# Kernel optimization log

Hardware: AMD Instinct MI355X
Metric: run time of the kernel (lower is better)

Reference implementation:

```python
import jax, jax.numpy as jnp
import numpy as np

EMBED_DIM = 1024
TASK_BIAS_DIM = 128
BATCH = 4
SEQ = 2048


def setup_inputs() -> dict:
    key = jax.random.key(0)
    kq, kk, kv, kt, kw, kb = jax.random.split(key, 6)
    query = jax.random.normal(kq, (BATCH, SEQ, EMBED_DIM), dtype=jnp.float32)
    key_t = jax.random.normal(kk, (BATCH, SEQ, EMBED_DIM), dtype=jnp.float32)
    value = jax.random.normal(kv, (BATCH, SEQ, EMBED_DIM), dtype=jnp.float32)
    task_bias = jax.random.normal(kt, (BATCH, TASK_BIAS_DIM), dtype=jnp.float32)
    # task_bias_proj: Linear(task_bias_dim, 1) -> weight [1, task_bias_dim], bias [1]
    lim = 1.0 / np.sqrt(TASK_BIAS_DIM)
    W = jax.random.uniform(kw, (TASK_BIAS_DIM, 1), jnp.float32, -lim, lim)
    b = jax.random.uniform(kb, (1,), jnp.float32, -lim, lim)
    return {"query": query, "key": key_t, "value": value,
            "task_bias": task_bias, "W": W, "b": b}


def reference(query, key, value, task_bias, W, b):
    scale = EMBED_DIM ** 0.5
    # scores: [batch, seq, seq]
    scores = jnp.einsum('bqd,bkd->bqk', query, key) / scale
    # per-batch scalar gate from task bias: [batch, 1]
    gate = jax.nn.sigmoid(task_bias @ W + b)           # [batch, 1]
    scores = scores * gate[:, :, None]                 # broadcast [b,1,1]
    attention_weights = jax.nn.softmax(scores, axis=-1)
    output = jnp.einsum('bqk,bkd->bqd', attention_weights, value)
    return output, attention_weights
```

## Files before the change

### kernel.cpp

```cpp
#include <hip/hip_runtime.h>
#include <hip/hip_bf16.h>
#include <stdint.h>
#include <stddef.h>

#define B_  4
#define S_  2048
#define D_  1024
#define TB_ 128

typedef float v4f  __attribute__((ext_vector_type(4)));
typedef short s16x4 __attribute__((ext_vector_type(4)));
typedef short s16x8 __attribute__((ext_vector_type(8)));

#define WAITV(n) asm volatile("s_waitcnt vmcnt(" #n ")" ::: "memory")

__device__ __forceinline__ unsigned short f2bf(float f) {
  union { float f; unsigned u; } x; x.f = f;
  unsigned u = x.u;
  unsigned r = (u + 0x7FFFu + ((u >> 16) & 1u)) >> 16;
  return (unsigned short)r;
}

__device__ __forceinline__ void gld16(const void* g, void* l) {
  __builtin_amdgcn_global_load_lds(
      (const __attribute__((address_space(1))) unsigned int*)g,
      (__attribute__((address_space(3))) unsigned int*)l, 16, 0, 0);
}

__device__ __forceinline__ void barrier_sync() {
  asm volatile("" ::: "memory");
  __builtin_amdgcn_s_barrier();
  asm volatile("" ::: "memory");
  __builtin_amdgcn_sched_barrier(0);
}

__global__ __launch_bounds__(256) void gate_kernel(
    const float* __restrict__ tb, const float* __restrict__ W,
    const float* __restrict__ bias, float* __restrict__ gate) {
  int t = threadIdx.x;
  int b = t >> 6, l = t & 63;
  float s = tb[b * TB_ + l] * W[l] + tb[b * TB_ + 64 + l] * W[64 + l];
  #pragma unroll
  for (int off = 32; off > 0; off >>= 1) s += __shfl_down(s, off, 64);
  if (l == 0) gate[b] = 1.0f / (1.0f + __expf(-(s + bias[0])));
}

__global__ __launch_bounds__(256) void cvt_bf16_kernel(
    const float* __restrict__ src, short* __restrict__ dst) {
  size_t g = (size_t)blockIdx.x * 256 + threadIdx.x;
  v4f v = *(const v4f*)(src + g * 4);
  s16x4 o;
  o[0] = (short)f2bf(v[0]); o[1] = (short)f2bf(v[1]);
  o[2] = (short)f2bf(v[2]); o[3] = (short)f2bf(v[3]);
  *(s16x4*)(dst + g * 4) = o;
}

__global__ __launch_bounds__(256) void vT_kernel(
    const float* __restrict__ V, short* __restrict__ VT) {
  __shared__ float tile[64][65];
  int b = blockIdx.z;
  int s0 = blockIdx.x * 64, d0 = blockIdx.y * 64;
  int t = threadIdx.x;
  int tc = t & 63, tr4 = t >> 6;
  const float* src = V + ((size_t)b * S_ + s0) * D_ + d0;
  #pragma unroll
  for (int p = 0; p < 16; ++p) {
    int r = p * 4 + tr4;
    tile[r][tc] = src[(size_t)r * D_ + tc];
  }
  __syncthreads();
  short* dst = VT + ((size_t)b * D_ + d0) * S_ + s0;
  #pragma unroll
  for (int p = 0; p < 16; ++p) {
    int r = p * 4 + tr4;
    dst[(size_t)r * S_ + tc] = (short)f2bf(tile[tc][r]);
  }
}

template<int BN, int KTOT, int BROWS, int LDC, bool GATED>
__global__ __launch_bounds__(512, 2) void gemm_pipe(
    const short* __restrict__ Ag, const short* __restrict__ Bg,
    const float* __restrict__ gate, float* __restrict__ Cg) {
  extern __shared__ char lds[];
  constexpr int NF = BN / 64;
  constexpr int NT = KTOT / 64;
  constexpr int ABYTES = 256 * 128;
  constexpr int BBYTES = BN * 128;
  constexpr int BUFB = ABYTES + BBYTES;

  int wg = blockIdx.x;
  int swz = (wg & 7) * 32 + (wg >> 3);
  int b = swz >> 6;
  int rem = swz & 63;
  int m0 = (rem >> 3) * 256;
  int n0 = (rem & 7) * BN;

  int tid = threadIdx.x;
  int w = tid >> 6, l = tid & 63;
  int wm = w >> 2, wn = w & 3;

  const short* Ab = Ag + (size_t)b * S_ * KTOT + (size_t)m0 * KTOT;
  const short* Bb = Bg + (size_t)b * BROWS * KTOT + (size_t)n0 * KTOT;

  int srow8 = l >> 3;
  int schunk = ((l & 7) ^ srow8) * 8;

  int arow = wm * 128 + (l & 15);
  int brow = wn * (BN / 4) + (l & 15);
  int hi = l >> 4;
  int sl0 = (((0 + hi) ^ (l & 7)) * 16);
  int sl1 = (((4 + hi) ^ (l & 7)) * 16);

  v4f acc[8][NF];
  #pragma unroll
  for (int m = 0; m < 8; ++m)
    #pragma unroll
    for (int n = 0; n < NF; ++n)
      #pragma unroll
      for (int j = 0; j < 4; ++j) acc[m][n][j] = 0.0f;

  auto stage = [&](int t, int buf) {
    char* La = lds + buf * BUFB;
    char* Lb = La + ABYTES;
    const short* As = Ab + (size_t)t * 64 + schunk;
    #pragma unroll
    for (int j = 0; j < 4; ++j) {
      int blk = w * 4 + j;
      gld16(As + (size_t)(blk * 8 + srow8) * KTOT, La + blk * 1024);
    }
    const short* Bs = Bb + (size_t)t * 64 + schunk;
    #pragma unroll
    for (int j = 0; j < NF; ++j) {
      int blk = w * NF + j;
      gld16(Bs + (size_t)(blk * 8 + srow8) * KTOT, Lb + blk * 1024);
    }
  };

  auto compute = [&](int buf) {
    const char* La = lds + buf * BUFB + arow * 128;
    const char* Lb = lds + buf * BUFB + ABYTES + brow * 128;
    s16x8 bf0[NF], bf1[NF];
    #pragma unroll
    for (int n = 0; n < NF; ++n) {
      bf0[n] = *(const s16x8*)(Lb + n * 2048 + sl0);
      bf1[n] = *(const s16x8*)(Lb + n * 2048 + sl1);
    }
    #pragma unroll
    for (int mh = 0; mh < 2; ++mh) {
      s16x8 af[4];
      #pragma unroll
      for (int i = 0; i < 4; ++i)
        af[i] = *(const s16x8*)(La + (mh * 4 + i) * 2048 + sl0);
      __builtin_amdgcn_s_setprio(1);
      #pragma unroll
      for (int i = 0; i < 4; ++i)
        #pragma unroll
        for (int n = 0; n < NF; ++n)
          acc[mh * 4 + i][n] = __builtin_amdgcn_mfma_f32_16x16x32_bf16(
              af[i], bf0[n], acc[mh * 4 + i][n], 0, 0, 0);
      __builtin_amdgcn_s_setprio(0);
      #pragma unroll
      for (int i = 0; i < 4; ++i)
        af[i] = *(const s16x8*)(La + (mh * 4 + i) * 2048 + sl1);
      __builtin_amdgcn_s_setprio(1);
      #pragma unroll
      for (int i = 0; i < 4; ++i)
        #pragma unroll
        for (int n = 0; n < NF; ++n)
          acc[mh * 4 + i][n] = __builtin_amdgcn_mfma_f32_16x16x32_bf16(
              af[i], bf1[n], acc[mh * 4 + i][n], 0, 0, 0);
      __builtin_amdgcn_s_setprio(0);
    }
  };

  stage(0, 0);
  int cur = 0;
  for (int t = 0; t < NT - 1; ++t) {
    stage(t + 1, cur ^ 1);
    if constexpr (BN == 256) { WAITV(8); } else { WAITV(6); }
    barrier_sync();
    compute(cur);
    barrier_sync();
    cur ^= 1;
  }
  WAITV(0);
  barrier_sync();
  compute(cur);

  float g = 1.0f;
  if constexpr (GATED) g = gate[b] * 0.03125f;
  float* Cb = Cg + (size_t)b * S_ * LDC +
              (size_t)(m0 + wm * 128) * LDC + n0 + wn * (BN / 4);
  #pragma unroll
  for (int mf = 0; mf < 8; ++mf)
    #pragma unroll
    for (int n = 0; n < NF; ++n) {
      int r0 = mf * 16 + hi * 4;
      int c = n * 16 + (l & 15);
      #pragma unroll
      for (int j = 0; j < 4; ++j)
        Cb[(size_t)(r0 + j) * LDC + c] = acc[mf][n][j] * g;
    }
}

__global__ __launch_bounds__(256) void softmax_kernel(
    float* __restrict__ attn, short* __restrict__ attnb) {
  size_t row = blockIdx.x;
  float* p = attn + row * S_;
  int t = threadIdx.x;
  v4f v0 = *(const v4f*)(p + t * 8);
  v4f v1 = *(const v4f*)(p + t * 8 + 4);
  float m = fmaxf(fmaxf(fmaxf(v0[0], v0[1]), fmaxf(v0[2], v0[3])),
                  fmaxf(fmaxf(v1[0], v1[1]), fmaxf(v1[2], v1[3])));
  #pragma unroll
  for (int off = 32; off > 0; off >>= 1) m = fmaxf(m, __shfl_xor(m, off, 64));
  __shared__ float rm[4], rs[4];
  if ((t & 63) == 0) rm[t >> 6] = m;
  __syncthreads();
  m = fmaxf(fmaxf(rm[0], rm[1]), fmaxf(rm[2], rm[3]));
  float e[8]; float sum = 0.0f;
  #pragma unroll
  for (int j = 0; j < 4; ++j) { e[j] = __expf(v0[j] - m); sum += e[j]; }
  #pragma unroll
  for (int j = 0; j < 4; ++j) { e[4 + j] = __expf(v1[j] - m); sum += e[4 + j]; }
  #pragma unroll
  for (int off = 32; off > 0; off >>= 1) sum += __shfl_xor(sum, off, 64);
  if ((t & 63) == 0) rs[t >> 6] = sum;
  __syncthreads();
  sum = rs[0] + rs[1] + rs[2] + rs[3];
  float inv = 1.0f / sum;
  #pragma unroll
  for (int j = 0; j < 4; ++j) v0[j] = e[j] * inv;
  #pragma unroll
  for (int j = 0; j < 4; ++j) v1[j] = e[4 + j] * inv;
  *(v4f*)(p + t * 8) = v0;
  *(v4f*)(p + t * 8 + 4) = v1;
  s16x8 ob;
  ob[0] = (short)f2bf(v0[0]); ob[1] = (short)f2bf(v0[1]);
  ob[2] = (short)f2bf(v0[2]); ob[3] = (short)f2bf(v0[3]);
  ob[4] = (short)f2bf(v1[0]); ob[5] = (short)f2bf(v1[1]);
  ob[6] = (short)f2bf(v1[2]); ob[7] = (short)f2bf(v1[3]);
  *(s16x8*)(attnb + row * S_ + t * 8) = ob;
}

extern "C" void kernel_launch(void* const* d_in, const int* in_sizes, int n_in,
                              void* d_out, int out_size, void* d_ws, size_t ws_size,
                              hipStream_t stream) {
  (void)in_sizes; (void)n_in; (void)out_size; (void)ws_size;
  const float* Q  = (const float*)d_in[0];
  const float* K  = (const float*)d_in[1];
  const float* V  = (const float*)d_in[2];
  const float* tb = (const float*)d_in[3];
  const float* W  = (const float*)d_in[4];
  const float* bias = (const float*)d_in[5];

  float* out  = (float*)d_out;
  float* attn = out + (size_t)B_ * S_ * D_;

  char* ws = (char*)d_ws;
  float* gate = (float*)ws;
  short* Qb = (short*)(ws + 256);
  short* Kb = Qb + (size_t)B_ * S_ * D_;
  short* VT = Kb + (size_t)B_ * S_ * D_;
  short* attnb = Qb;

  auto* qkf = gemm_pipe<256, 1024, 2048, 2048, true>;
  auto* pvf = gemm_pipe<128, 2048, 1024, 1024, false>;
  constexpr int QK_LDS = 2 * (256 + 256) * 64 * 2;
  constexpr int PV_LDS = 2 * (256 + 128) * 64 * 2;
  (void)hipFuncSetAttribute((const void*)qkf,
      hipFuncAttributeMaxDynamicSharedMemorySize, QK_LDS);
  (void)hipFuncSetAttribute((const void*)pvf,
      hipFuncAttributeMaxDynamicSharedMemorySize, PV_LDS);

  gate_kernel<<<1, 256, 0, stream>>>(tb, W, bias, gate);
  cvt_bf16_kernel<<<8192, 256, 0, stream>>>(Q, Qb);
  cvt_bf16_kernel<<<8192, 256, 0, stream>>>(K, Kb);
  vT_kernel<<<dim3(32, 16, 4), 256, 0, stream>>>(V, VT);
  qkf<<<256, 512, QK_LDS, stream>>>(Qb, Kb, gate, attn);
  softmax_kernel<<<8192, 256, 0, stream>>>(attn, attnb);
  pvf<<<256, 512, PV_LDS, stream>>>(attnb, VT, gate, out);
}
```

Measured before the change: 140.4 us.

## Restructure GEMM mainloop into 4-buffer K=32 pipeline with split A/B staging

Rewrites the bf16 MFMA GEMM mainloop to use K-steps of 32 with a 4-deep LDS ring buffer and three tiles in flight. A and B loads for future tiles are issued separately in two half-phases interleaved with MFMA work. The PV GEMM now uses a different wave layout (4x2 waves, 4 m-fragments each). The aim is to hide global-load latency and LDS-read latency better. In exchange it adds more barriers per K step and a new swizzle pattern whose bank-conflict behaviour is unverified.

```diff
diff --git a/kernel.cpp b/kernel.cpp
--- a/kernel.cpp
+++ b/kernel.cpp
@@ -13,6 +13,16 @@
 typedef short s16x8 __attribute__((ext_vector_type(8)));
 
 #define WAITV(n) asm volatile("s_waitcnt vmcnt(" #n ")" ::: "memory")
+#define LGKM0 do { asm volatile("s_waitcnt lgkmcnt(0)" ::: "memory"); \
+                   __builtin_amdgcn_sched_barrier(0); } while (0)
+
+template<int N> __device__ __forceinline__ void waitvT() {
+  if constexpr (N == 0) WAITV(0);
+  else if constexpr (N == 3) WAITV(3);
+  else if constexpr (N == 4) WAITV(4);
+  else if constexpr (N == 6) WAITV(6);
+  else if constexpr (N == 8) WAITV(8);
+}
 
 __device__ __forceinline__ unsigned short f2bf(float f) {
   union { float f; unsigned u; } x; x.f = f;
@@ -77,126 +87,123 @@
   }
 }
 
-template<int BN, int KTOT, int BROWS, int LDC, bool GATED>
+template<int MF, int WNC, int BLOADS, int KT, int BROWS, int LDC, bool GATED>
 __global__ __launch_bounds__(512, 2) void gemm_pipe(
     const short* __restrict__ Ag, const short* __restrict__ Bg,
     const float* __restrict__ gate, float* __restrict__ Cg) {
   extern __shared__ char lds[];
-  constexpr int NF = BN / 64;
-  constexpr int NT = KTOT / 64;
-  constexpr int ABYTES = 256 * 128;
-  constexpr int BBYTES = BN * 128;
+  constexpr int NF = 4;
+  constexpr int PH_MF = MF / 2;
+  constexpr int NT = KT / 32;
+  constexpr int ABYTES = 256 * 64;
+  constexpr int BROWS_T = WNC * NF * 16;
+  constexpr int BBYTES = BROWS_T * 64;
   constexpr int BUFB = ABYTES + BBYTES;
+  constexpr int LSTEADY = 2 * (2 + BLOADS);
+  constexpr int LP1 = 2 + BLOADS;
 
   int wg = blockIdx.x;
   int swz = (wg & 7) * 32 + (wg >> 3);
   int b = swz >> 6;
   int rem = swz & 63;
   int m0 = (rem >> 3) * 256;
-  int n0 = (rem & 7) * BN;
+  int n0 = (rem & 7) * BROWS_T;
 
   int tid = threadIdx.x;
   int w = tid >> 6, l = tid & 63;
-  int wm = w >> 2, wn = w & 3;
-
-  const short* Ab = Ag + (size_t)b * S_ * KTOT + (size_t)m0 * KTOT;
-  const short* Bb = Bg + (size_t)b * BROWS * KTOT + (size_t)n0 * KTOT;
-
-  int srow8 = l >> 3;
-  int schunk = ((l & 7) ^ srow8) * 8;
-
-  int arow = wm * 128 + (l & 15);
-  int brow = wn * (BN / 4) + (l & 15);
+  int wm = w / WNC, wn = w % WNC;
+
+  const short* Ab = Ag + (size_t)b * S_ * KT + (size_t)m0 * KT;
+  const short* Bb = Bg + (size_t)b * BROWS * KT + (size_t)n0 * KT;
+
+  int tid4 = tid >> 2;
+  int slog8 = ((tid & 3) ^ ((tid >> 3) & 3)) * 8;
+  int fr = l & 15;
   int hi = l >> 4;
-  int sl0 = (((0 + hi) ^ (l & 7)) * 16);
-  int sl1 = (((4 + hi) ^ (l & 7)) * 16);
-
-  v4f acc[8][NF];
-  #pragma unroll
-  for (int m = 0; m < 8; ++m)
+  int sl16 = (hi ^ ((l >> 1) & 3)) * 16;
+
+  v4f acc[MF][NF];
+  #pragma unroll
+  for (int m = 0; m < MF; ++m)
     #pragma unroll
     for (int n = 0; n < NF; ++n)
       #pragma unroll
       for (int j = 0; j < 4; ++j) acc[m][n][j] = 0.0f;
 
-  auto stage = [&](int t, int buf) {
-    char* La = lds + buf * BUFB;
-    char* Lb = La + ABYTES;
-    const short* As = Ab + (size_t)t * 64 + schunk;
-    #pragma unroll
-    for (int j = 0; j < 4; ++j) {
-      int blk = w * 4 + j;
-      gld16(As + (size_t)(blk * 8 + srow8) * KTOT, La + blk * 1024);
-    }
-    const short* Bs = Bb + (size_t)t * 64 + schunk;
-    #pragma unroll
-    for (int j = 0; j < NF; ++j) {
-      int blk = w * NF + j;
-      gld16(Bs + (size_t)(blk * 8 + srow8) * KTOT, Lb + blk * 1024);
-    }
+  auto stageA = [&](int tt) {
+    char* La = lds + (tt & 3) * BUFB;
+    const short* src = Ab + (size_t)tid4 * KT + tt * 32 + slog8;
+    gld16(src, La + tid * 16);
+    gld16(src + (size_t)128 * KT, La + 8192 + tid * 16);
   };
-
-  auto compute = [&](int buf) {
-    const char* La = lds + buf * BUFB + arow * 128;
-    const char* Lb = lds + buf * BUFB + ABYTES + brow * 128;
-    s16x8 bf0[NF], bf1[NF];
-    #pragma unroll
-    for (int n = 0; n < NF; ++n) {
-      bf0[n] = *(const s16x8*)(Lb + n * 2048 + sl0);
-      bf1[n] = *(const s16x8*)(Lb + n * 2048 + sl1);
-    }
-    #pragma unroll
-    for (int mh = 0; mh < 2; ++mh) {
-      s16x8 af[4];
-      #pragma unroll
-      for (int i = 0; i < 4; ++i)
-        af[i] = *(const s16x8*)(La + (mh * 4 + i) * 2048 + sl0);
+  auto stageB = [&](int tt) {
+    char* Lb = lds + (tt & 3) * BUFB + ABYTES;
+    const short* src = Bb + (size_t)tid4 * KT + tt * 32 + slog8;
+    gld16(src, Lb + tid * 16);
+    if constexpr (BLOADS == 2)
+      gld16(src + (size_t)128 * KT, Lb + 8192 + tid * 16);
+  };
+
+  stageA(0); stageB(0); stageA(1); stageB(1); stageA(2); stageB(2);
+
+  s16x8 bf[NF];
+  for (int t = 0; t < NT; ++t) {
+    if (t < NT - 2) waitvT<LSTEADY>();
+    else if (t == NT - 2) waitvT<LP1>();
+    else waitvT<0>();
+    barrier_sync();
+    const char* base = lds + (t & 3) * BUFB;
+    {
+      #pragma unroll
+      for (int n = 0; n < NF; ++n)
+        bf[n] = *(const s16x8*)(base + ABYTES +
+                 (size_t)(wn * 64 + n * 16 + fr) * 64 + sl16);
+      s16x8 af[PH_MF];
+      #pragma unroll
+      for (int i = 0; i < PH_MF; ++i)
+        af[i] = *(const s16x8*)(base +
+                 (size_t)(wm * MF * 16 + i * 16 + fr) * 64 + sl16);
+      if (t + 3 < NT) stageA(t + 3);
+      LGKM0;
       __builtin_amdgcn_s_setprio(1);
       #pragma unroll
-      for (int i = 0; i < 4; ++i)
+      for (int i = 0; i < PH_MF; ++i)
         #pragma unroll
         for (int n = 0; n < NF; ++n)
-          acc[mh * 4 + i][n] = __builtin_amdgcn_mfma_f32_16x16x32_bf16(
-              af[i], bf0[n], acc[mh * 4 + i][n], 0, 0, 0);
+          acc[i][n] = __builtin_amdgcn_mfma_f32_16x16x32_bf16(
+              af[i], bf[n], acc[i][n], 0, 0, 0);
       __builtin_amdgcn_s_setprio(0);
-      #pragma unroll
-      for (int i = 0; i < 4; ++i)
-        af[i] = *(const s16x8*)(La + (mh * 4 + i) * 2048 + sl1);
+    }
+    barrier_sync();
+    {
+      s16x8 af[PH_MF];
+      #pragma unroll
+      for (int i = 0; i < PH_MF; ++i)
+        af[i] = *(const s16x8*)(base +
+                 (size_t)(wm * MF * 16 + (PH_MF + i) * 16 + fr) * 64 + sl16);
+      if (t + 3 < NT) stageB(t + 3);
+      LGKM0;
       __builtin_amdgcn_s_setprio(1);
       #pragma unroll
-      for (int i = 0; i < 4; ++i)
+      for (int i = 0; i < PH_MF; ++i)
         #pragma unroll
         for (int n = 0; n < NF; ++n)
-          acc[mh * 4 + i][n] = __builtin_amdgcn_mfma_f32_16x16x32_bf16(
-              af[i], bf1[n], acc[mh * 4 + i][n], 0, 0, 0);
+          acc[PH_MF + i][n] = __builtin_amdgcn_mfma_f32_16x16x32_bf16(
+              af[i], bf[n], acc[PH_MF + i][n], 0, 0, 0);
       __builtin_amdgcn_s_setprio(0);
     }
-  };
-
-  stage(0, 0);
-  int cur = 0;
-  for (int t = 0; t < NT - 1; ++t) {
-    stage(t + 1, cur ^ 1);
-    if constexpr (BN == 256) { WAITV(8); } else { WAITV(6); }
-    barrier_sync();
-    compute(cur);
-    barrier_sync();
-    cur ^= 1;
   }
-  WAITV(0);
-  barrier_sync();
-  compute(cur);
 
   float g = 1.0f;
   if constexpr (GATED) g = gate[b] * 0.03125f;
   float* Cb = Cg + (size_t)b * S_ * LDC +
-              (size_t)(m0 + wm * 128) * LDC + n0 + wn * (BN / 4);
-  #pragma unroll
-  for (int mf = 0; mf < 8; ++mf)
+              (size_t)(m0 + wm * MF * 16) * LDC + n0 + wn * 64;
+  #pragma unroll
+  for (int mf = 0; mf < MF; ++mf)
     #pragma unroll
     for (int n = 0; n < NF; ++n) {
       int r0 = mf * 16 + hi * 4;
-      int c = n * 16 + (l & 15);
+      int c = n * 16 + fr;
       #pragma unroll
       for (int j = 0; j < 4; ++j)
         Cb[(size_t)(r0 + j) * LDC + c] = acc[mf][n][j] * g;
@@ -264,10 +271,10 @@
   short* VT = Kb + (size_t)B_ * S_ * D_;
   short* attnb = Qb;
 
-  auto* qkf = gemm_pipe<256, 1024, 2048, 2048, true>;
-  auto* pvf = gemm_pipe<128, 2048, 1024, 1024, false>;
-  constexpr int QK_LDS = 2 * (256 + 256) * 64 * 2;
-  constexpr int PV_LDS = 2 * (256 + 128) * 64 * 2;
+  auto* qkf = gemm_pipe<8, 4, 2, 1024, 2048, 2048, true>;
+  auto* pvf = gemm_pipe<4, 2, 1, 2048, 1024, 1024, false>;
+  constexpr int QK_LDS = 4 * (16384 + 16384);
+  constexpr int PV_LDS = 4 * (16384 + 8192);
   (void)hipFuncSetAttribute((const void*)qkf,
       hipFuncAttributeMaxDynamicSharedMemorySize, QK_LDS);
   (void)hipFuncSetAttribute((const void*)pvf,
```

After: 143.8 us. +2.5%, slower.

## Reshape GEMM wave tiling and prefetch A fragments across compute phases

Applied to the files above, without the earlier changes.

The bf16 MFMA GEMM template is reparameterised by per-wave M fragments and wave-column count. The PV GEMM now uses a 4x2 wave grid where each wave owns a 64x64 tile, instead of a 128x32 strip, which improves operand reuse per LDS read. The inner loop is restructured into phases of two M fragments, with the next phase's A fragments prefetched into registers while the current MFMAs run. This adds extra block barriers inside each K tile, which may cost more synchronisation than the overlap saves.

```diff
diff --git a/kernel.cpp b/kernel.cpp
--- a/kernel.cpp
+++ b/kernel.cpp
@@ -77,13 +77,15 @@
   }
 }
 
-template<int BN, int KTOT, int BROWS, int LDC, bool GATED>
+template<int MF, int WNC, int BLOADS, int KT, int BROWS, int LDC, bool GATED>
 __global__ __launch_bounds__(512, 2) void gemm_pipe(
     const short* __restrict__ Ag, const short* __restrict__ Bg,
     const float* __restrict__ gate, float* __restrict__ Cg) {
   extern __shared__ char lds[];
-  constexpr int NF = BN / 64;
-  constexpr int NT = KTOT / 64;
+  constexpr int NF = 4;
+  constexpr int PH = MF / 2;
+  constexpr int NT = KT / 64;
+  constexpr int BN = WNC * 64;
   constexpr int ABYTES = 256 * 128;
   constexpr int BBYTES = BN * 128;
   constexpr int BUFB = ABYTES + BBYTES;
@@ -97,23 +99,21 @@
 
   int tid = threadIdx.x;
   int w = tid >> 6, l = tid & 63;
-  int wm = w >> 2, wn = w & 3;
-
-  const short* Ab = Ag + (size_t)b * S_ * KTOT + (size_t)m0 * KTOT;
-  const short* Bb = Bg + (size_t)b * BROWS * KTOT + (size_t)n0 * KTOT;
+  int wm = w / WNC, wn = w % WNC;
+
+  const short* Ab = Ag + (size_t)b * S_ * KT + (size_t)m0 * KT;
+  const short* Bb = Bg + (size_t)b * BROWS * KT + (size_t)n0 * KT;
 
   int srow8 = l >> 3;
   int schunk = ((l & 7) ^ srow8) * 8;
-
-  int arow = wm * 128 + (l & 15);
-  int brow = wn * (BN / 4) + (l & 15);
+  int fr = l & 15;
   int hi = l >> 4;
-  int sl0 = (((0 + hi) ^ (l & 7)) * 16);
-  int sl1 = (((4 + hi) ^ (l & 7)) * 16);
-
-  v4f acc[8][NF];
-  #pragma unroll
-  for (int m = 0; m < 8; ++m)
+  int sl0 = ((hi) ^ (l & 7)) * 16;
+  int sl1 = ((4 + hi) ^ (l & 7)) * 16;
+
+  v4f acc[MF][NF];
+  #pragma unroll
+  for (int m = 0; m < MF; ++m)
     #pragma unroll
     for (int n = 0; n < NF; ++n)
       #pragma unroll
@@ -126,77 +126,84 @@
     #pragma unroll
     for (int j = 0; j < 4; ++j) {
       int blk = w * 4 + j;
-      gld16(As + (size_t)(blk * 8 + srow8) * KTOT, La + blk * 1024);
+      gld16(As + (size_t)(blk * 8 + srow8) * KT, La + blk * 1024);
     }
     const short* Bs = Bb + (size_t)t * 64 + schunk;
     #pragma unroll
-    for (int j = 0; j < NF; ++j) {
-      int blk = w * NF + j;
-      gld16(Bs + (size_t)(blk * 8 + srow8) * KTOT, Lb + blk * 1024);
+    for (int j = 0; j < BLOADS; ++j) {
+      int blk = w * BLOADS + j;
+      gld16(Bs + (size_t)(blk * 8 + srow8) * KT, Lb + blk * 1024);
     }
   };
 
-  auto compute = [&](int buf) {
-    const char* La = lds + buf * BUFB + arow * 128;
-    const char* Lb = lds + buf * BUFB + ABYTES + brow * 128;
-    s16x8 bf0[NF], bf1[NF];
+  stage(0, 0);
+  int cur = 0;
+  for (int t = 0; t < NT; ++t) {
+    if (t + 1 < NT) {
+      stage(t + 1, cur ^ 1);
+      if constexpr (BLOADS == 4) WAITV(8); else WAITV(6);
+    } else {
+      WAITV(0);
+    }
+    barrier_sync();
+    const char* base = lds + cur * BUFB;
+    const char* Bbase = base + ABYTES;
+    s16x8 bfr[NF][2];
     #pragma unroll
     for (int n = 0; n < NF; ++n) {
-      bf0[n] = *(const s16x8*)(Lb + n * 2048 + sl0);
-      bf1[n] = *(const s16x8*)(Lb + n * 2048 + sl1);
-    }
-    #pragma unroll
-    for (int mh = 0; mh < 2; ++mh) {
-      s16x8 af[4];
-      #pragma unroll
-      for (int i = 0; i < 4; ++i)
-        af[i] = *(const s16x8*)(La + (mh * 4 + i) * 2048 + sl0);
+      const char* rp = Bbase + (size_t)(wn * 64 + n * 16 + fr) * 128;
+      bfr[n][0] = *(const s16x8*)(rp + sl0);
+      bfr[n][1] = *(const s16x8*)(rp + sl1);
+    }
+    s16x8 afc[2][2];
+    #pragma unroll
+    for (int i = 0; i < 2; ++i) {
+      const char* rp = base + (size_t)(wm * (MF * 16) + i * 16 + fr) * 128;
+      afc[i][0] = *(const s16x8*)(rp + sl0);
+      afc[i][1] = *(const s16x8*)(rp + sl1);
+    }
+    barrier_sync();
+    #pragma unroll
+    for (int p = 0; p < PH; ++p) {
+      s16x8 afn[2][2];
+      if (p + 1 < PH) {
+        #pragma unroll
+        for (int i = 0; i < 2; ++i) {
+          const char* rp = base +
+              (size_t)(wm * (MF * 16) + (2 * (p + 1) + i) * 16 + fr) * 128;
+          afn[i][0] = *(const s16x8*)(rp + sl0);
+          afn[i][1] = *(const s16x8*)(rp + sl1);
+        }
+      }
       __builtin_amdgcn_s_setprio(1);
       #pragma unroll
-      for (int i = 0; i < 4; ++i)
+      for (int kh = 0; kh < 2; ++kh)
         #pragma unroll
-        for (int n = 0; n < NF; ++n)
-          acc[mh * 4 + i][n] = __builtin_amdgcn_mfma_f32_16x16x32_bf16(
-              af[i], bf0[n], acc[mh * 4 + i][n], 0, 0, 0);
+        for (int i = 0; i < 2; ++i)
+          #pragma unroll
+          for (int n = 0; n < NF; ++n)
+            acc[2 * p + i][n] = __builtin_amdgcn_mfma_f32_16x16x32_bf16(
+                afc[i][kh], bfr[n][kh], acc[2 * p + i][n], 0, 0, 0);
       __builtin_amdgcn_s_setprio(0);
-      #pragma unroll
-      for (int i = 0; i < 4; ++i)
-        af[i] = *(const s16x8*)(La + (mh * 4 + i) * 2048 + sl1);
-      __builtin_amdgcn_s_setprio(1);
-      #pragma unroll
-      for (int i = 0; i < 4; ++i)
-        #pragma unroll
-        for (int n = 0; n < NF; ++n)
-          acc[mh * 4 + i][n] = __builtin_amdgcn_mfma_f32_16x16x32_bf16(
-              af[i], bf1[n], acc[mh * 4 + i][n], 0, 0, 0);
-      __builtin_amdgcn_s_setprio(0);
-    }
-  };
-
-  stage(0, 0);
-  int cur = 0;
-  for (int t = 0; t < NT - 1; ++t) {
-    stage(t + 1, cur ^ 1);
-    if constexpr (BN == 256) { WAITV(8); } else { WAITV(6); }
-    barrier_sync();
-    compute(cur);
-    barrier_sync();
+      if (p + 1 < PH) {
+        afc[0][0] = afn[0][0]; afc[0][1] = afn[0][1];
+        afc[1][0] = afn[1][0]; afc[1][1] = afn[1][1];
+      }
+      barrier_sync();
+    }
     cur ^= 1;
   }
-  WAITV(0);
-  barrier_sync();
-  compute(cur);
 
   float g = 1.0f;
   if constexpr (GATED) g = gate[b] * 0.03125f;
   float* Cb = Cg + (size_t)b * S_ * LDC +
-              (size_t)(m0 + wm * 128) * LDC + n0 + wn * (BN / 4);
-  #pragma unroll
-  for (int mf = 0; mf < 8; ++mf)
+              (size_t)(m0 + wm * (MF * 16)) * LDC + n0 + wn * 64;
+  #pragma unroll
+  for (int mf = 0; mf < MF; ++mf)
     #pragma unroll
     for (int n = 0; n < NF; ++n) {
       int r0 = mf * 16 + hi * 4;
-      int c = n * 16 + (l & 15);
+      int c = n * 16 + fr;
       #pragma unroll
       for (int j = 0; j < 4; ++j)
         Cb[(size_t)(r0 + j) * LDC + c] = acc[mf][n][j] * g;
@@ -264,8 +271,8 @@
   short* VT = Kb + (size_t)B_ * S_ * D_;
   short* attnb = Qb;
 
-  auto* qkf = gemm_pipe<256, 1024, 2048, 2048, true>;
-  auto* pvf = gemm_pipe<128, 2048, 1024, 1024, false>;
+  auto* qkf = gemm_pipe<8, 4, 4, 1024, 2048, 2048, true>;
+  auto* pvf = gemm_pipe<4, 2, 2, 2048, 1024, 1024, false>;
   constexpr int QK_LDS = 2 * (256 + 256) * 64 * 2;
   constexpr int PV_LDS = 2 * (256 + 128) * 64 * 2;
   (void)hipFuncSetAttribute((const void*)qkf,
```

Measured after the change: 142.1 us. About the same (+1.2%).
